# Performance work log

Measured on AMD Instinct MI355X. Metric: run time of the kernel, lower is better.

The kernel has to match this reference:

```python
import jax, jax.numpy as jnp
import numpy as np

NUM_TAGS = 9
INNER_DIM = 64
HIDDEN = 768
MASK_VAL = 1e12


def setup_inputs() -> dict:
    key = jax.random.key(0)
    k1, k2, k3, k4 = jax.random.split(key, 4)
    B, S = 16, 512
    encoder_output = jax.random.normal(k1, (B, S, HIDDEN), dtype=jnp.float32)
    token_ids = jax.random.randint(k2, (B, S), 0, 30000, dtype=jnp.int64)
    attention_mask = jnp.ones((B, S), dtype=jnp.int32)
    W = jax.random.normal(k3, (HIDDEN, NUM_TAGS * INNER_DIM * 2), dtype=jnp.float32) * 0.02
    b = jax.random.normal(k4, (NUM_TAGS * INNER_DIM * 2,), dtype=jnp.float32) * 0.02
    return {"encoder_output": encoder_output, "token_ids": token_ids,
            "attention_mask": attention_mask, "W": W, "b": b}


def _rope_sin_cos(seq_len, dim, dtype):
    # sinusoidal position embedding, interleaved then repeat_interleave(2)
    pos = jnp.arange(seq_len, dtype=dtype)[:, None]              # [S,1]
    inv = jnp.power(10000.0, -2.0 * jnp.arange(dim // 2, dtype=dtype) / dim)
    ang = pos * inv                                              # [S,d/2]
    sin = jnp.repeat(jnp.sin(ang), 2, axis=-1)                   # [S,d]
    cos = jnp.repeat(jnp.cos(ang), 2, axis=-1)                   # [S,d]
    return sin, cos


def _rotate_half(x):
    # stack([-x[...,1::2], x[...,::2]], -1).reshape(x.shape)
    x2 = jnp.stack([-x[..., 1::2], x[..., ::2]], axis=-1)
    return x2.reshape(x.shape)


def reference(encoder_output, token_ids, attention_mask, W, b):
    B, S, _ = encoder_output.shape
    d = INNER_DIM
    out = encoder_output @ W + b                                 # [B,S,T*2d]
    out = out.reshape(B, S, NUM_TAGS, 2 * d)
    qw, kw = out[..., :d], out[..., d:]                          # [B,S,T,d]

    sin, cos = _rope_sin_cos(S, d, encoder_output.dtype)
    sin = sin[None, :, None, :]                                  # [1,S,1,d]
    cos = cos[None, :, None, :]
    qw = qw * cos + _rotate_half(qw) * sin
    kw = kw * cos + _rotate_half(kw) * sin

    logits = jnp.einsum('bshd,bthd->bhst', qw, kw)               # [B,T,S,S]

    pad = attention_mask.astype(logits.dtype)[:, None, None, :]  # key-side mask
    logits = logits * pad - (1.0 - pad) * MASK_VAL
    tril = jnp.tril(jnp.ones((S, S), dtype=logits.dtype), -1)
    logits = logits - tril * MASK_VAL
    return logits / jnp.sqrt(jnp.asarray(d, logits.dtype))
```

## Files before the change

kernel.cpp:

```cpp
#include <hip/hip_runtime.h>

#define MASK_VALF 1000000000000.0f

typedef __attribute__((ext_vector_type(8))) short s16x8;
typedef __attribute__((ext_vector_type(4))) float f32x4;
typedef __attribute__((ext_vector_type(16))) float f32x16;

__device__ __forceinline__ unsigned f2bf_u(float f) {
    union { float f; unsigned u; } v; v.f = f;
    return (v.u + 0x7FFFu + ((v.u >> 16) & 1u)) >> 16;
}
__device__ __forceinline__ short f2bf(float f) { return (short)(f2bf_u(f) & 0xFFFFu); }

#define GLOAD16(gp, lp) __builtin_amdgcn_global_load_lds( \
    (const __attribute__((address_space(1))) void*)(gp),  \
    (__attribute__((address_space(3))) void*)(lp), 16, 0, 0)

__global__ __launch_bounds__(256) void prep_all(
    const float* __restrict__ enc, short* __restrict__ encb,
    const float* __restrict__ W, short* __restrict__ wtb,
    float* __restrict__ scf)
{
    const int blk = blockIdx.x;
    const int t = threadIdx.x;
    if (blk < 6144) {
        int i = blk * 256 + t;
        float4 v = ((const float4*)enc)[i];
        short4 o;
        o.x = f2bf(v.x); o.y = f2bf(v.y); o.z = f2bf(v.z); o.w = f2bf(v.w);
        ((short4*)encb)[i] = o;
    } else if (blk < 7008) {
        __shared__ float tile[32][33];
        int tb = blk - 6144;
        int tbx = tb % 36;
        int tby = tb / 36;
        int tx = t & 31, ty = t >> 5;
#pragma unroll
        for (int r = 0; r < 4; ++r) {
            int row = ty + r * 8;
            tile[row][tx] = W[(tby * 32 + row) * 1152 + tbx * 32 + tx];
        }
        __syncthreads();
#pragma unroll
        for (int r = 0; r < 4; ++r) {
            int row = ty + r * 8;
            wtb[(size_t)(tbx * 32 + row) * 768 + tby * 32 + tx] = f2bf(tile[tx][row]);
        }
    } else {
        int id = (blk - 7008) * 256 + t;
        int pos = id >> 5, j = id & 31;
        float inv = powf(10000.0f, -2.0f * (float)j / 64.0f);
        float ang = (float)pos * inv;
        float s, c;
        sincosf(ang, &s, &c);
        scf[id * 2]     = c;
        scf[id * 2 + 1] = s;
    }
}

__global__ __launch_bounds__(256) void gemm1_rope(
    const short* __restrict__ A,
    const short* __restrict__ Bt,
    const float* __restrict__ bias,
    const float* __restrict__ scf,
    short* __restrict__ qk)
{
    __shared__ __align__(16) short As[2][128 * 32];
    __shared__ __align__(16) short Bs[2][128 * 32];
    const int t = threadIdx.x;
    const int w = t >> 6, lane = t & 63;
    const int l31 = lane & 31, lh = lane >> 5;
    const int wn2 = w & 1, wm2 = w >> 1;
    const int m0 = blockIdx.y * 128;
    const int n0 = blockIdx.x * 128;

    f32x16 acc[2][2] = {};

    const int srow = t >> 2;
    const int scol = (t & 3) ^ (srow & 3);
    const short* gA = A  + (size_t)(m0 + srow) * 768 + scol * 8;
    const short* gB = Bt + (size_t)(n0 + srow) * 768 + scol * 8;

    GLOAD16(gA,            &As[0][w * 512]);
    GLOAD16(gA + 64 * 768, &As[0][2048 + w * 512]);
    GLOAD16(gB,            &Bs[0][w * 512]);
    GLOAD16(gB + 64 * 768, &Bs[0][2048 + w * 512]);
    gA += 32; gB += 32;

    auto compute = [&](const short* as, const short* bs) {
        s16x8 af[2][2], bf[2][2];
        const int swz = l31 & 3;
#pragma unroll
        for (int fi = 0; fi < 2; ++fi)
#pragma unroll
            for (int kk = 0; kk < 2; ++kk) {
                const int ca = (kk * 2 + lh) ^ swz;
                af[fi][kk] = *(const s16x8*)&bs[(wn2 * 64 + fi * 32 + l31) * 32 + ca * 8];
                bf[fi][kk] = *(const s16x8*)&as[(wm2 * 64 + fi * 32 + l31) * 32 + ca * 8];
            }
#pragma unroll
        for (int kk = 0; kk < 2; ++kk)
#pragma unroll
            for (int fi = 0; fi < 2; ++fi)
#pragma unroll
                for (int fj = 0; fj < 2; ++fj)
                    acc[fi][fj] = __builtin_amdgcn_mfma_f32_32x32x16_bf16(
                        af[fi][kk], bf[fj][kk], acc[fi][fj], 0, 0, 0);
    };

    for (int kt = 0; kt < 23; ++kt) {
        __syncthreads();
        const int cur = kt & 1, nxt = cur ^ 1;
        GLOAD16(gA,            &As[nxt][w * 512]);
        GLOAD16(gA + 64 * 768, &As[nxt][2048 + w * 512]);
        GLOAD16(gB,            &Bs[nxt][w * 512]);
        GLOAD16(gB + 64 * 768, &Bs[nxt][2048 + w * 512]);
        gA += 32; gB += 32;
        compute(As[cur], Bs[cur]);
    }
    __syncthreads();
    compute(As[1], Bs[1]);

#pragma unroll
    for (int fi = 0; fi < 2; ++fi) {
        const int n_base = n0 + wn2 * 64 + fi * 32;
#pragma unroll
        for (int fj = 0; fj < 2; ++fj) {
            const int rowg = m0 + wm2 * 64 + fj * 32 + l31;
            const int bidx = rowg >> 9;
            const int pos  = rowg & 511;
#pragma unroll
            for (int g = 0; g < 4; ++g) {
                const int colg0 = n_base + g * 8 + lh * 4;
                const float4 bv = *(const float4*)&bias[colg0];
                const int tag = colg0 >> 7;
                const int qkf = (colg0 >> 6) & 1;
                const int dd0 = colg0 & 63;
                const float4 cs = *(const float4*)&scf[pos * 64 + dd0];
                float x0 = acc[fi][fj][g * 4 + 0] + bv.x;
                float x1 = acc[fi][fj][g * 4 + 1] + bv.y;
                float x2 = acc[fi][fj][g * 4 + 2] + bv.z;
                float x3 = acc[fi][fj][g * 4 + 3] + bv.w;
                float o0 = x0 * cs.x - x1 * cs.y;
                float o1 = x1 * cs.x + x0 * cs.y;
                float o2 = x2 * cs.z - x3 * cs.w;
                float o3 = x3 * cs.z + x2 * cs.w;
                int2 st;
                st.x = (int)(f2bf_u(o0) & 0xFFFFu) | (int)(f2bf_u(o1) << 16);
                st.y = (int)(f2bf_u(o2) & 0xFFFFu) | (int)(f2bf_u(o3) << 16);
                *(int2*)&qk[((((size_t)bidx * 9 + tag) * 2 + qkf) * 512 + pos) * 64 + dd0] = st;
            }
        }
    }
}

__global__ __launch_bounds__(256) void gemm2_mask(
    const short* __restrict__ qk,
    const int* __restrict__ amask,
    float* __restrict__ out)
{
    const int t = threadIdx.x;
    const int w = t >> 6, lane = t & 63;
    const int lr = lane & 15, quad = lane >> 4;
    const int wm = w >> 1, wn = w & 1;
    const int bh = blockIdx.z;
    const int bidx = bh / 9;
    const int s0 = blockIdx.y * 128;
    const int t0 = blockIdx.x * 128;

    const short* qbase = qk + (size_t)bh * 2 * 512 * 64;
    const short* kbase = qbase + 512 * 64;

    s16x8 af[2][4], bw[2][4];
#pragma unroll
    for (int kk = 0; kk < 2; ++kk) {
#pragma unroll
        for (int i = 0; i < 4; ++i)
            af[kk][i] = *(const s16x8*)&kbase[(size_t)(t0 + wm * 64 + i * 16 + lr) * 64 + kk * 32 + quad * 8];
#pragma unroll
        for (int j = 0; j < 4; ++j)
            bw[kk][j] = *(const s16x8*)&qbase[(size_t)(s0 + wn * 64 + j * 16 + lr) * 64 + kk * 32 + quad * 8];
    }

    f32x4 acc[4][4] = {};
#pragma unroll
    for (int kk = 0; kk < 2; ++kk)
#pragma unroll
        for (int i = 0; i < 4; ++i)
#pragma unroll
            for (int j = 0; j < 4; ++j)
                acc[i][j] = __builtin_amdgcn_mfma_f32_16x16x32_bf16(af[kk][i], bw[kk][j], acc[i][j], 0, 0, 0);

#pragma unroll
    for (int i = 0; i < 4; ++i) {
        const int tg0 = t0 + wm * 64 + i * 16 + quad * 4;
        const int4 am = *(const int4*)&amask[bidx * 512 + tg0];
        const float4 pad = make_float4((float)am.x, (float)am.y, (float)am.z, (float)am.w);
        const float4 mk = make_float4((1.0f - pad.x) * MASK_VALF, (1.0f - pad.y) * MASK_VALF,
                                      (1.0f - pad.z) * MASK_VALF, (1.0f - pad.w) * MASK_VALF);
#pragma unroll
        for (int j = 0; j < 4; ++j) {
            const int sg = s0 + wn * 64 + j * 16 + lr;
            float4 v;
            v.x = (acc[i][j][0] * pad.x - mk.x - (sg > tg0     ? MASK_VALF : 0.0f)) * 0.125f;
            v.y = (acc[i][j][1] * pad.y - mk.y - (sg > tg0 + 1 ? MASK_VALF : 0.0f)) * 0.125f;
            v.z = (acc[i][j][2] * pad.z - mk.z - (sg > tg0 + 2 ? MASK_VALF : 0.0f)) * 0.125f;
            v.w = (acc[i][j][3] * pad.w - mk.w - (sg > tg0 + 3 ? MASK_VALF : 0.0f)) * 0.125f;
            *(float4*)&out[((size_t)bh * 512 + sg) * 512 + tg0] = v;
        }
    }
}

extern "C" void kernel_launch(void* const* d_in, const int* in_sizes, int n_in,
                              void* d_out, int out_size, void* d_ws, size_t ws_size,
                              hipStream_t stream) {
    const float* enc   = (const float*)d_in[0];
    const int*   amask = (const int*)d_in[2];
    const float* W     = (const float*)d_in[3];
    const float* bias  = (const float*)d_in[4];
    float* out = (float*)d_out;

    char* ws = (char*)d_ws;
    short* encb = (short*)(ws);
    short* wtb  = (short*)(ws + 12582912);
    float* scf  = (float*)(ws + 14352384);
    short* qk   = (short*)(ws + 14483456);

    prep_all  <<<7072, 256, 0, stream>>>(enc, encb, W, wtb, scf);
    gemm1_rope<<<dim3(9, 64), 256, 0, stream>>>(encb, wtb, bias, scf, qk);
    gemm2_mask<<<dim3(4, 4, 144), 256, 0, stream>>>(qk, amask, out);
}
```

Baseline: 236.0 us.

## Load GEMM1 operands directly from global into registers, dropping LDS staging

The projection GEMM no longer stages A/B tiles through shared memory with global_load_lds and barriers. Each wave now reads its MFMA fragments straight from global memory into a register double buffer, with a launch-bounds occupancy hint added. This removes the LDS traffic and __syncthreads, but waves in a block sharing rows now each fetch those tiles themselves instead of reusing one shared copy. The loads are narrow strided 16-byte reads per lane, which puts more pressure on cache and global bandwidth.

Result: slower. 274.9 us (+16.5%).

```diff
diff --git a/kernel.cpp b/kernel.cpp
--- a/kernel.cpp
+++ b/kernel.cpp
@@ -11,10 +11,6 @@
     return (v.u + 0x7FFFu + ((v.u >> 16) & 1u)) >> 16;
 }
 __device__ __forceinline__ short f2bf(float f) { return (short)(f2bf_u(f) & 0xFFFFu); }
-
-#define GLOAD16(gp, lp) __builtin_amdgcn_global_load_lds( \
-    (const __attribute__((address_space(1))) void*)(gp),  \
-    (__attribute__((address_space(3))) void*)(lp), 16, 0, 0)
 
 __global__ __launch_bounds__(256) void prep_all(
     const float* __restrict__ enc, short* __restrict__ encb,
@@ -58,15 +54,13 @@
     }
 }
 
-__global__ __launch_bounds__(256) void gemm1_rope(
+__global__ __launch_bounds__(256, 3) void gemm1_rope(
     const short* __restrict__ A,
     const short* __restrict__ Bt,
     const float* __restrict__ bias,
     const float* __restrict__ scf,
     short* __restrict__ qk)
 {
-    __shared__ __align__(16) short As[2][128 * 32];
-    __shared__ __align__(16) short Bs[2][128 * 32];
     const int t = threadIdx.x;
     const int w = t >> 6, lane = t & 63;
     const int l31 = lane & 31, lh = lane >> 5;
@@ -76,28 +70,36 @@
 
     f32x16 acc[2][2] = {};
 
-    const int srow = t >> 2;
-    const int scol = (t & 3) ^ (srow & 3);
-    const short* gA = A  + (size_t)(m0 + srow) * 768 + scol * 8;
-    const short* gB = Bt + (size_t)(n0 + srow) * 768 + scol * 8;
-
-    GLOAD16(gA,            &As[0][w * 512]);
-    GLOAD16(gA + 64 * 768, &As[0][2048 + w * 512]);
-    GLOAD16(gB,            &Bs[0][w * 512]);
-    GLOAD16(gB + 64 * 768, &Bs[0][2048 + w * 512]);
-    gA += 32; gB += 32;
-
-    auto compute = [&](const short* as, const short* bs) {
-        s16x8 af[2][2], bf[2][2];
-        const int swz = l31 & 3;
-#pragma unroll
-        for (int fi = 0; fi < 2; ++fi)
-#pragma unroll
-            for (int kk = 0; kk < 2; ++kk) {
-                const int ca = (kk * 2 + lh) ^ swz;
-                af[fi][kk] = *(const s16x8*)&bs[(wn2 * 64 + fi * 32 + l31) * 32 + ca * 8];
-                bf[fi][kk] = *(const s16x8*)&as[(wm2 * 64 + fi * 32 + l31) * 32 + ca * 8];
-            }
+    const short* pA[2];
+    const short* pB[2];
+#pragma unroll
+    for (int fi = 0; fi < 2; ++fi)
+        pA[fi] = Bt + (size_t)(n0 + wn2 * 64 + fi * 32 + l31) * 768 + lh * 8;
+#pragma unroll
+    for (int fj = 0; fj < 2; ++fj)
+        pB[fj] = A + (size_t)(m0 + wm2 * 64 + fj * 32 + l31) * 768 + lh * 8;
+
+    s16x8 af[2][2][2], bf[2][2][2];
+#pragma unroll
+    for (int fi = 0; fi < 2; ++fi)
+#pragma unroll
+        for (int kk = 0; kk < 2; ++kk) {
+            af[0][fi][kk] = *(const s16x8*)(pA[fi] + kk * 16);
+            bf[0][fi][kk] = *(const s16x8*)(pB[fi] + kk * 16);
+        }
+
+    for (int kt = 0; kt < 24; ++kt) {
+        const int cur = kt & 1, nxt = cur ^ 1;
+        if (kt < 23) {
+            const int off = (kt + 1) * 32;
+#pragma unroll
+            for (int fi = 0; fi < 2; ++fi)
+#pragma unroll
+                for (int kk = 0; kk < 2; ++kk) {
+                    af[nxt][fi][kk] = *(const s16x8*)(pA[fi] + off + kk * 16);
+                    bf[nxt][fi][kk] = *(const s16x8*)(pB[fi] + off + kk * 16);
+                }
+        }
 #pragma unroll
         for (int kk = 0; kk < 2; ++kk)
 #pragma unroll
@@ -105,21 +107,8 @@
 #pragma unroll
                 for (int fj = 0; fj < 2; ++fj)
                     acc[fi][fj] = __builtin_amdgcn_mfma_f32_32x32x16_bf16(
-                        af[fi][kk], bf[fj][kk], acc[fi][fj], 0, 0, 0);
-    };
-
-    for (int kt = 0; kt < 23; ++kt) {
-        __syncthreads();
-        const int cur = kt & 1, nxt = cur ^ 1;
-        GLOAD16(gA,            &As[nxt][w * 512]);
-        GLOAD16(gA + 64 * 768, &As[nxt][2048 + w * 512]);
-        GLOAD16(gB,            &Bs[nxt][w * 512]);
-        GLOAD16(gB + 64 * 768, &Bs[nxt][2048 + w * 512]);
-        gA += 32; gB += 32;
-        compute(As[cur], Bs[cur]);
-    }
-    __syncthreads();
-    compute(As[1], Bs[1]);
+                        af[cur][fi][kk], bf[cur][fj][kk], acc[fi][fj], 0, 0, 0);
+    }
 
 #pragma unroll
     for (int fi = 0; fi < 2; ++fi) {
```
